# Optimization experiments

Hardware: AMD Instinct MI355X
Metric: run time of the kernel (lower is better)

Reference implementation:

```python
import jax, jax.numpy as jnp
import numpy as np

B = 32768      # batch
S = 512        # state_dim
G = 128        # goal_dim
A = 32         # action_dim
P = 16         # num_primitives
H1, H2 = 512, 256        # big_model hidden sizes
VH1, VH2 = 1024, 512     # value hidden sizes


def _w(k, shape, scale=0.05):
    return jax.random.normal(k, shape, jnp.float32) * scale


def setup_inputs() -> dict:
    key = jax.random.key(0)
    ks = jax.random.split(key, 24)
    d = {"features": jax.random.normal(ks[0], (B, S + G), jnp.float32)}
    # state encoder: S->H1->H2
    d["se_w1"] = _w(ks[1], (S, H1));  d["se_b1"] = jnp.zeros((H1,), jnp.float32)
    d["se_w2"] = _w(ks[2], (H1, H2)); d["se_b2"] = jnp.zeros((H2,), jnp.float32)
    # goal encoder: G->H1->H2
    d["ge_w1"] = _w(ks[3], (G, H1));  d["ge_b1"] = jnp.zeros((H1,), jnp.float32)
    d["ge_w2"] = _w(ks[4], (H1, H2)); d["ge_b2"] = jnp.zeros((H2,), jnp.float32)
    # gate: 2*H2->H2->P (sigmoid)
    d["gt_w1"] = _w(ks[5], (2 * H2, H2)); d["gt_b1"] = jnp.zeros((H2,), jnp.float32)
    d["gt_w2"] = _w(ks[6], (H2, P));      d["gt_b2"] = jnp.zeros((P,), jnp.float32)
    # primitive state encoder: S->H1->H2
    d["pse_w1"] = _w(ks[7], (S, H1));  d["pse_b1"] = jnp.zeros((H1,), jnp.float32)
    d["pse_w2"] = _w(ks[8], (H1, H2)); d["pse_b2"] = jnp.zeros((H2,), jnp.float32)
    # P primitives, each H2->H2->2A (stacked for batched GEMM)
    d["pw1"] = _w(ks[9], (P, H2, H2));     d["pb1"] = jnp.zeros((P, H2), jnp.float32)
    d["pw2"] = _w(ks[10], (P, H2, 2 * A)); d["pb2"] = jnp.zeros((P, 2 * A), jnp.float32)
    # value net: (S+G)->VH1->VH2
    d["vf_w1"] = _w(ks[11], (S + G, VH1)); d["vf_b1"] = jnp.zeros((VH1,), jnp.float32)
    d["vf_w2"] = _w(ks[12], (VH1, VH2));   d["vf_b2"] = jnp.zeros((VH2,), jnp.float32)
    return d


def _mlp2(x, w1, b1, w2, b2):
    return jax.nn.relu(jax.nn.relu(x @ w1 + b1) @ w2 + b2)


def reference(features,
              se_w1, se_b1, se_w2, se_b2,
              ge_w1, ge_b1, ge_w2, ge_b2,
              gt_w1, gt_b1, gt_w2, gt_b2,
              pse_w1, pse_b1, pse_w2, pse_b2,
              pw1, pb1, pw2, pb2,
              vf_w1, vf_b1, vf_w2, vf_b2):
    state, goal = features[:, :S], features[:, S:]
    # gating weights
    s_emb = _mlp2(state, se_w1, se_b1, se_w2, se_b2)      # [B,H2]
    g_emb = _mlp2(goal, ge_w1, ge_b1, ge_w2, ge_b2)       # [B,H2]
    gate_in = jnp.concatenate([s_emb, g_emb], axis=-1)    # [B,2*H2]
    weights = jax.nn.sigmoid(jax.nn.relu(gate_in @ gt_w1 + gt_b1) @ gt_w2 + gt_b2)  # [B,P]
    # shared primitive embedding
    prim_embed = _mlp2(state, pse_w1, pse_b1, pse_w2, pse_b2)  # [B,H2]
    # all primitives as one batched GEMM
    h = jax.nn.relu(jnp.einsum('bh,phk->bpk', prim_embed, pw1) + pb1[None])  # [B,P,H2]
    out = jnp.einsum('bpk,pkd->bpd', h, pw2) + pb2[None]                      # [B,P,2A]
    mu, log_std = out[..., :A], out[..., A:]
    sigma = jnp.exp(log_std)
    # precision-weighted Gaussian mixture
    inv = weights[..., None] / sigma        # [B,P,A]
    denom = inv.sum(axis=1)                 # [B,A]
    mean = (inv * mu).sum(axis=1) / denom   # [B,A]  (learn_log_std=True -> mean only)
    # critic
    value = _mlp2(features, vf_w1, vf_b1, vf_w2, vf_b2)  # [B,VH2]
    return (mean, value)
```

## Files before the change

kernel.cpp:

```cpp
#include <hip/hip_runtime.h>
#include <stdint.h>

#define NB 32768

typedef __bf16 bf16x8 __attribute__((ext_vector_type(8)));
typedef float f32x4 __attribute__((ext_vector_type(4)));

__device__ __forceinline__ unsigned pack_bf2(float a, float b) {
  union { __bf16 h[2]; unsigned u; } t;
  t.h[0] = (__bf16)a; t.h[1] = (__bf16)b;
  return t.u;
}
__device__ __forceinline__ unsigned short bf16b(float f) {
  union { __bf16 h; unsigned short u; } t;
  t.h = (__bf16)f;
  return t.u;
}
__device__ __forceinline__ float bf2f(unsigned short h) {
  union { unsigned u; float f; } v; v.u = ((unsigned)h) << 16;
  return v.f;
}

__device__ __forceinline__ void gld_lds16(void* lds, const void* g) {
  __builtin_amdgcn_global_load_lds(
      (__attribute__((address_space(1))) unsigned int*)(uintptr_t)g,
      (__attribute__((address_space(3))) unsigned int*)(uintptr_t)lds,
      16, 0, 0);
}

__device__ __forceinline__ int xcd_swz(int bid, int nwg) {
  return (bid & 7) * (nwg >> 3) + (bid >> 3);
}


__global__ __launch_bounds__(256) void fconv_k(const float* __restrict__ src,
                                               unsigned short* __restrict__ dst) {
  size_t idx = ((size_t)blockIdx.x * 256 + threadIdx.x) * 8;
  float4 a = *(const float4*)(src + idx);
  float4 b = *(const float4*)(src + idx + 4);
  uint4 o;
  o.x = pack_bf2(a.x, a.y); o.y = pack_bf2(a.z, a.w);
  o.z = pack_bf2(b.x, b.y); o.w = pack_bf2(b.z, b.w);
  *(uint4*)(dst + idx) = o;
}

__global__ __launch_bounds__(256) void bcat_k(const float* __restrict__ a,
                                              const float* __restrict__ b,
                                              float* __restrict__ dst) {
  const int i = blockIdx.x * 256 + threadIdx.x;
  dst[i] = (i < 512) ? a[i] : b[i - 512];
}

struct TJobs {
  const float* src[11];
  unsigned short* dst[11];
  int K[11], N[11], batch[11];
};

__global__ __launch_bounds__(256) void wtrans_k(TJobs jobs) {
  const int job = blockIdx.y;
  const int K = jobs.K[job], N = jobs.N[job];
  const int KT = K >> 5, NT = N >> 5;
  const int ntiles = jobs.batch[job] * KT * NT;
  const int t = blockIdx.x;
  if (t >= ntiles) return;
  const int b = t / (KT * NT);
  const int rem = t - b * KT * NT;
  const int kt = rem / NT, nt = rem - kt * NT;
  const float* src = jobs.src[job] + (size_t)b * K * N;
  unsigned short* dst = jobs.dst[job] + (size_t)b * K * N;
  __shared__ float tile[32][33];
  const int i = threadIdx.x >> 5, jj = threadIdx.x & 31;
#pragma unroll
  for (int s = 0; s < 4; ++s)
    tile[i + 8 * s][jj] = src[(size_t)(kt * 32 + i + 8 * s) * N + nt * 32 + jj];
  __syncthreads();
#pragma unroll
  for (int s = 0; s < 4; ++s)
    dst[(size_t)(nt * 32 + i + 8 * s) * K + kt * 32 + jj] = bf16b(tile[jj][i + 8 * s]);
}


template <bool OUT_BF16>
__global__ __launch_bounds__(256, 2) void gemm2_k(const unsigned short* __restrict__ A, int lda,
                                                  const unsigned short* __restrict__ WT,
                                                  const float* __restrict__ bias,
                                                  void* __restrict__ Cout, int ldc, int K,
                                                  int ncl2) {
  __shared__ unsigned short a_s[2][128 * 32];
  __shared__ unsigned short b_s[2][256 * 32];
  const int tid = threadIdx.x;
  const int l = tid & 63, w = tid >> 6;
  const int lr = l & 15, lq = l >> 4;
  const int wg = xcd_swz(blockIdx.x, gridDim.x);
  const int col0 = (wg & ((1 << ncl2) - 1)) << 8;
  const int row0 = (wg >> ncl2) << 7;
  const int wbase = tid & ~63;

  auto stage = [&](int buf, int t) {
    const int k0 = t << 5;
#pragma unroll
    for (int i = 0; i < 2; ++i) {
      const int s = i * 256 + tid;
      const int r = s >> 2, c = s & 3;
      const int cs = c ^ ((r >> 1) & 3);
      gld_lds16(&a_s[buf][(size_t)(i * 256 + wbase) * 8],
                A + (size_t)(row0 + r) * lda + k0 + cs * 8);
    }
#pragma unroll
    for (int i = 0; i < 4; ++i) {
      const int s = i * 256 + tid;
      const int n = s >> 2, c = s & 3;
      const int cs = c ^ ((n >> 1) & 3);
      gld_lds16(&b_s[buf][(size_t)(i * 256 + wbase) * 8],
                WT + (size_t)(col0 + n) * K + k0 + cs * 8);
    }
  };

  f32x4 acc[8][4] = {};
  const int nt = K >> 5;
  stage(0, 0);
  __syncthreads();
#pragma unroll 1
  for (int t = 0; t < nt; ++t) {
    const int cur = t & 1;
    if (t + 1 < nt) stage(cur ^ 1, t + 1);
    bf16x8 av[8], bv[4];
#pragma unroll
    for (int mf = 0; mf < 8; ++mf) {
      const int r = mf * 16 + lr;
      av[mf] = *(const bf16x8*)&a_s[cur][r * 32 + ((lq ^ ((r >> 1) & 3)) << 3)];
    }
#pragma unroll
    for (int nf = 0; nf < 4; ++nf) {
      const int n = w * 64 + nf * 16 + lr;
      bv[nf] = *(const bf16x8*)&b_s[cur][n * 32 + ((lq ^ ((n >> 1) & 3)) << 3)];
    }
#pragma unroll
    for (int mf = 0; mf < 8; ++mf)
#pragma unroll
      for (int nf = 0; nf < 4; ++nf)
        acc[mf][nf] = __builtin_amdgcn_mfma_f32_16x16x32_bf16(av[mf], bv[nf], acc[mf][nf], 0, 0, 0);
    __syncthreads();
  }

#pragma unroll
  for (int nf = 0; nf < 4; ++nf) {
    const int gc = col0 + w * 64 + nf * 16 + lr;
    const float bb = bias[gc];
#pragma unroll
    for (int mf = 0; mf < 8; ++mf) {
      const int gr = row0 + mf * 16 + (lq << 2);
#pragma unroll
      for (int r = 0; r < 4; ++r) {
        float v = acc[mf][nf][r] + bb;
        v = fmaxf(v, 0.0f);
        if (OUT_BF16)
          ((unsigned short*)Cout)[(size_t)(gr + r) * ldc + gc] = bf16b(v);
        else
          ((float*)Cout)[(size_t)(gr + r) * ldc + gc] = v;
      }
    }
  }
}


template <bool OUT_BF16>
__global__ __launch_bounds__(256, 2) void gemm3_k(const unsigned short* __restrict__ A, int lda,
                                                  const unsigned short* __restrict__ WT,
                                                  const float* __restrict__ bias,
                                                  void* __restrict__ Cout, int ldc, int K,
                                                  int ncl2) {
  __shared__ unsigned short a_s[2][128 * 32];
  __shared__ unsigned short b_s[2][128 * 32];
  const int tid = threadIdx.x;
  const int l = tid & 63, w = tid >> 6;
  const int wm = w >> 1, wn = w & 1;
  const int lr = l & 15, lq = l >> 4;
  const int wg = xcd_swz(blockIdx.x, gridDim.x);
  const int col0 = (wg & ((1 << ncl2) - 1)) << 7;
  const int row0 = (wg >> ncl2) << 7;
  const int wbase = tid & ~63;

  auto stage = [&](int buf, int t) {
    const int k0 = t << 5;
#pragma unroll
    for (int i = 0; i < 2; ++i) {
      const int s = i * 256 + tid;
      const int r = s >> 2, c = s & 3;
      const int cs = c ^ ((r >> 1) & 3);
      gld_lds16(&a_s[buf][(size_t)(i * 256 + wbase) * 8],
                A + (size_t)(row0 + r) * lda + k0 + cs * 8);
    }
#pragma unroll
    for (int i = 0; i < 2; ++i) {
      const int s = i * 256 + tid;
      const int n = s >> 2, c = s & 3;
      const int cs = c ^ ((n >> 1) & 3);
      gld_lds16(&b_s[buf][(size_t)(i * 256 + wbase) * 8],
                WT + (size_t)(col0 + n) * K + k0 + cs * 8);
    }
  };

  f32x4 acc[4][4] = {};
  const int nt = K >> 5;
  stage(0, 0);
  __syncthreads();
#pragma unroll 1
  for (int t = 0; t < nt; ++t) {
    const int cur = t & 1;
    if (t + 1 < nt) stage(cur ^ 1, t + 1);
    bf16x8 av[4], bv[4];
#pragma unroll
    for (int mf = 0; mf < 4; ++mf) {
      const int r = wm * 64 + mf * 16 + lr;
      av[mf] = *(const bf16x8*)&a_s[cur][r * 32 + ((lq ^ ((r >> 1) & 3)) << 3)];
    }
#pragma unroll
    for (int nf = 0; nf < 4; ++nf) {
      const int n = wn * 64 + nf * 16 + lr;
      bv[nf] = *(const bf16x8*)&b_s[cur][n * 32 + ((lq ^ ((n >> 1) & 3)) << 3)];
    }
#pragma unroll
    for (int mf = 0; mf < 4; ++mf)
#pragma unroll
      for (int nf = 0; nf < 4; ++nf)
        acc[mf][nf] = __builtin_amdgcn_mfma_f32_16x16x32_bf16(av[mf], bv[nf], acc[mf][nf], 0, 0, 0);
    __syncthreads();
  }

#pragma unroll
  for (int nf = 0; nf < 4; ++nf) {
    const int gc = col0 + wn * 64 + nf * 16 + lr;
    const float bb = bias[gc];
#pragma unroll
    for (int mf = 0; mf < 4; ++mf) {
      const int gr = row0 + wm * 64 + mf * 16 + (lq << 2);
#pragma unroll
      for (int r = 0; r < 4; ++r) {
        float v = acc[mf][nf][r] + bb;
        v = fmaxf(v, 0.0f);
        if (OUT_BF16)
          ((unsigned short*)Cout)[(size_t)(gr + r) * ldc + gc] = bf16b(v);
        else
          ((float*)Cout)[(size_t)(gr + r) * ldc + gc] = v;
      }
    }
  }
}


__global__ __launch_bounds__(256) void gt2_k(const unsigned short* __restrict__ gate_h,
                                             const float* __restrict__ w2,
                                             const float* __restrict__ b2,
                                             float* __restrict__ wgt) {
  __shared__ float w_s[256 * 16];
  __shared__ unsigned short a_s[16 * 264];
  const int tid = threadIdx.x;
  const int row0 = blockIdx.x * 16;
  for (int i = tid; i < 256 * 16; i += 256) w_s[i] = w2[i];
  for (int i = tid; i < 512; i += 256) {
    const int r = i >> 5, cg = i & 31;
    *(uint4*)&a_s[r * 264 + cg * 8] =
        *(const uint4*)(gate_h + (size_t)(row0 + r) * 256 + cg * 8);
  }
  __syncthreads();
  const int rr = tid >> 4, col = tid & 15;
  float sum = b2[col];
#pragma unroll 8
  for (int k = 0; k < 256; ++k)
    sum += bf2f(a_s[rr * 264 + k]) * w_s[k * 16 + col];
  wgt[(size_t)(row0 + rr) * 16 + col] = 1.0f / (1.0f + __expf(-sum));
}


__global__ __launch_bounds__(512, 4) void prim_head_k(
    const unsigned short* __restrict__ prim,
    const float* __restrict__ wgt,
    const unsigned short* __restrict__ pw1t,
    const float* __restrict__ pb1,
    const unsigned short* __restrict__ pw2t,
    const float* __restrict__ pb2,
    unsigned short* __restrict__ outbuf)
{
  __shared__ unsigned short prim_s[2][128 * 32];
  __shared__ unsigned short w1_s[2][128 * 32];
  __shared__ unsigned short h_s[128 * 128];
  __shared__ unsigned short pw2_s[64 * 128];
  const int tid = threadIdx.x;
  const int l = tid & 63;
  const int w = tid >> 6;
  const int lr = l & 15, lq = l >> 4;
  const int wn2 = w & 1, wr2 = w >> 1;
  const int row0 = blockIdx.x << 7;
  const int p = blockIdx.y;
  const int wbase = tid & ~63;

  const unsigned short* w1p = pw1t + (size_t)p * 65536;
  const unsigned short* w2p = pw2t + (size_t)p * 16384;

  auto stage_ab = [&](int t) {
    const int buf = t & 1;
    const int k0 = (t & 7) << 5;
    const int nb2 = (t >> 3) << 7;
    const int rw = tid >> 2, kc = tid & 3;
    const int kcs = kc ^ ((rw >> 1) & 3);
    gld_lds16(&prim_s[buf][(size_t)wbase * 8],
              prim + (size_t)(row0 + rw) * 256 + k0 + kcs * 8);
    gld_lds16(&w1_s[buf][(size_t)wbase * 8],
              w1p + (size_t)(nb2 + rw) * 256 + k0 + kcs * 8);
  };
  auto stage_pw2 = [&](int half) {
    const int nbase = half << 7;
#pragma unroll
    for (int i = 0; i < 2; ++i) {
      const int c = i * 512 + tid;
      const int d = c >> 4, kc = c & 15;
      gld_lds16(&pw2_s[(size_t)(i * 512 + wbase) * 8],
                w2p + (size_t)d * 256 + nbase + ((kc ^ (d & 7)) << 3));
    }
  };

  stage_ab(0);
  stage_pw2(0);

  f32x4 acc2[2][2] = {};

  for (int half = 0; half < 2; ++half) {
    float4 pb1v[4];
#pragma unroll
    for (int nf = 0; nf < 4; ++nf)
      pb1v[nf] = *(const float4*)(pb1 + p * 256 + (half << 7) + wn2 * 64 + nf * 16 + (lq << 2));

    f32x4 acc1[4][2] = {};
#pragma unroll 1
    for (int ks = 0; ks < 8; ++ks) {
      const int t = (half << 3) + ks;
      const int cur = t & 1;
      asm volatile("s_waitcnt vmcnt(0)" ::: "memory");
      __builtin_amdgcn_s_barrier();
      if (t < 15) stage_ab(t + 1);
      bf16x8 av[4], bv[2];
#pragma unroll
      for (int nf = 0; nf < 4; ++nf) {
        const int n = wn2 * 64 + nf * 16 + lr;
        av[nf] = *(const bf16x8*)&w1_s[cur][n * 32 + ((lq ^ ((n >> 1) & 3)) << 3)];
      }
#pragma unroll
      for (int rf = 0; rf < 2; ++rf) {
        const int r = wr2 * 32 + rf * 16 + lr;
        bv[rf] = *(const bf16x8*)&prim_s[cur][r * 32 + ((lq ^ ((r >> 1) & 3)) << 3)];
      }
#pragma unroll
      for (int nf = 0; nf < 4; ++nf)
#pragma unroll
        for (int rf = 0; rf < 2; ++rf)
          acc1[nf][rf] = __builtin_amdgcn_mfma_f32_16x16x32_bf16(av[nf], bv[rf], acc1[nf][rf], 0, 0, 0);
    }

#pragma unroll
    for (int nf = 0; nf < 4; ++nf) {
      const int n0 = wn2 * 64 + nf * 16 + (lq << 2);
      const float4 bb = pb1v[nf];
#pragma unroll
      for (int rf = 0; rf < 2; ++rf) {
        const int row = wr2 * 32 + rf * 16 + lr;
        uint2 pk;
        pk.x = pack_bf2(fmaxf(acc1[nf][rf][0] + bb.x, 0.0f),
                        fmaxf(acc1[nf][rf][1] + bb.y, 0.0f));
        pk.y = pack_bf2(fmaxf(acc1[nf][rf][2] + bb.z, 0.0f),
                        fmaxf(acc1[nf][rf][3] + bb.w, 0.0f));
        *(uint2*)&h_s[row * 128 + (((n0 >> 3) ^ (row & 7)) << 3) + (n0 & 7)] = pk;
      }
    }
    asm volatile("s_waitcnt lgkmcnt(0)" ::: "memory");
    __builtin_amdgcn_s_barrier();

    {
      const int dmu = wn2 * 16;
      const int row_a = wr2 * 32;
#pragma unroll
      for (int kc8 = 0; kc8 < 4; ++kc8) {
        const int slot = ((kc8 << 2) + lq) ^ (lr & 7);
        const bf16x8 amu = *(const bf16x8*)&pw2_s[(dmu + lr) * 128 + (slot << 3)];
        const bf16x8 als = *(const bf16x8*)&pw2_s[(dmu + 32 + lr) * 128 + (slot << 3)];
        const bf16x8 b0 = *(const bf16x8*)&h_s[(row_a + lr) * 128 + (slot << 3)];
        const bf16x8 b1 = *(const bf16x8*)&h_s[(row_a + 16 + lr) * 128 + (slot << 3)];
        acc2[0][0] = __builtin_amdgcn_mfma_f32_16x16x32_bf16(amu, b0, acc2[0][0], 0, 0, 0);
        acc2[0][1] = __builtin_amdgcn_mfma_f32_16x16x32_bf16(als, b0, acc2[0][1], 0, 0, 0);
        acc2[1][0] = __builtin_amdgcn_mfma_f32_16x16x32_bf16(amu, b1, acc2[1][0], 0, 0, 0);
        acc2[1][1] = __builtin_amdgcn_mfma_f32_16x16x32_bf16(als, b1, acc2[1][1], 0, 0, 0);
      }
    }
    asm volatile("s_waitcnt lgkmcnt(0)" ::: "memory");
    __builtin_amdgcn_s_barrier();
    if (half == 0) stage_pw2(1);
  }

  {
    const int dmu = wn2 * 16;
    const int row_a = wr2 * 32;
    const int d0 = dmu + (lq << 2);
    const float4 b2mu = *(const float4*)(pb2 + p * 64 + d0);
    const float4 b2ls = *(const float4*)(pb2 + p * 64 + 32 + d0);
    const float wp0 = wgt[(size_t)(row0 + row_a + lr) * 16 + p];
    const float wp1 = wgt[(size_t)(row0 + row_a + 16 + lr) * 16 + p];
#pragma unroll
    for (int s = 0; s < 2; ++s) {
      const int row_g = row0 + row_a + s * 16 + lr;
      const float wp = s ? wp1 : wp0;
      unsigned short* ob = outbuf + ((size_t)row_g * 16 + p) * 64;
      const float mu0 = acc2[s][0][0] + b2mu.x, ls0 = acc2[s][1][0] + b2ls.x;
      const float mu1 = acc2[s][0][1] + b2mu.y, ls1 = acc2[s][1][1] + b2ls.y;
      const float mu2 = acc2[s][0][2] + b2mu.z, ls2 = acc2[s][1][2] + b2ls.z;
      const float mu3 = acc2[s][0][3] + b2mu.w, ls3 = acc2[s][1][3] + b2ls.w;
      const float iv0 = wp * __expf(-ls0), iv1 = wp * __expf(-ls1);
      const float iv2 = wp * __expf(-ls2), iv3 = wp * __expf(-ls3);
      uint2 nmp, ivp;
      nmp.x = pack_bf2(iv0 * mu0, iv1 * mu1);
      nmp.y = pack_bf2(iv2 * mu2, iv3 * mu3);
      ivp.x = pack_bf2(iv0, iv1);
      ivp.y = pack_bf2(iv2, iv3);
      *(uint2*)(ob + d0) = nmp;
      *(uint2*)(ob + 32 + d0) = ivp;
    }
  }
}


__global__ __launch_bounds__(256) void mix_finish_k(const unsigned short* __restrict__ buf,
                                                    float* __restrict__ mean_out) {
  const int gid = blockIdx.x * 256 + threadIdx.x;
  const int row = gid >> 3;
  const int a0 = (gid & 7) * 4;
  const unsigned short* rp = buf + (size_t)row * 1024;
  float nx = 0, ny = 0, nz = 0, nw = 0, dx = 0, dy = 0, dz = 0, dw = 0;
#pragma unroll
  for (int p = 0; p < 16; ++p) {
    const uint2 m = *(const uint2*)(rp + p * 64 + a0);
    const uint2 v = *(const uint2*)(rp + p * 64 + 32 + a0);
    nx += bf2f((unsigned short)(m.x & 0xffff)); ny += bf2f((unsigned short)(m.x >> 16));
    nz += bf2f((unsigned short)(m.y & 0xffff)); nw += bf2f((unsigned short)(m.y >> 16));
    dx += bf2f((unsigned short)(v.x & 0xffff)); dy += bf2f((unsigned short)(v.x >> 16));
    dz += bf2f((unsigned short)(v.y & 0xffff)); dw += bf2f((unsigned short)(v.y >> 16));
  }
  float4 res;
  res.x = nx / dx; res.y = ny / dy; res.z = nz / dz; res.w = nw / dw;
  *(float4*)(mean_out + (size_t)row * 32 + a0) = res;
}


extern "C" void kernel_launch(void* const* d_in, const int* in_sizes, int n_in,
                              void* d_out, int out_size, void* d_ws, size_t ws_size,
                              hipStream_t stream) {
  const float* features = (const float*)d_in[0];
  const float* se_w1 = (const float*)d_in[1];
  const float* se_b1 = (const float*)d_in[2];
  const float* se_w2 = (const float*)d_in[3];
  const float* se_b2 = (const float*)d_in[4];
  const float* ge_w1 = (const float*)d_in[5];
  const float* ge_b1 = (const float*)d_in[6];
  const float* ge_w2 = (const float*)d_in[7];
  const float* ge_b2 = (const float*)d_in[8];
  const float* gt_w1 = (const float*)d_in[9];
  const float* gt_b1 = (const float*)d_in[10];
  const float* gt_w2 = (const float*)d_in[11];
  const float* gt_b2 = (const float*)d_in[12];
  const float* pse_w1 = (const float*)d_in[13];
  const float* pse_b1 = (const float*)d_in[14];
  const float* pse_w2 = (const float*)d_in[15];
  const float* pse_b2 = (const float*)d_in[16];
  const float* pw1 = (const float*)d_in[17];
  const float* pb1 = (const float*)d_in[18];
  const float* pw2 = (const float*)d_in[19];
  const float* pb2 = (const float*)d_in[20];
  const float* vf_w1 = (const float*)d_in[21];
  const float* vf_b1 = (const float*)d_in[22];
  const float* vf_w2 = (const float*)d_in[23];
  const float* vf_b2 = (const float*)d_in[24];
  (void)in_sizes; (void)n_in; (void)out_size; (void)ws_size;

  char* base = (char*)d_ws;
  size_t off = 0;
  auto alloc = [&](size_t bytes) -> char* {
    char* p = base + off;
    off += (bytes + 255) & ~(size_t)255;
    return p;
  };
  unsigned short* fbf     = (unsigned short*)alloc((size_t)NB * 640 * 2);
  unsigned short* bufA    = (unsigned short*)alloc((size_t)NB * 1024 * 2);
  unsigned short* g1      = (unsigned short*)alloc((size_t)NB * 512 * 2);
  unsigned short* gate_in = (unsigned short*)alloc((size_t)NB * 512 * 2);
  unsigned short* gate_h  = (unsigned short*)alloc((size_t)NB * 256 * 2);
  unsigned short* prim    = (unsigned short*)alloc((size_t)NB * 256 * 2);
  float* wgt              = (float*)alloc((size_t)NB * 16 * 4);
  unsigned short* wcat1t  = (unsigned short*)alloc((size_t)1024 * 512 * 2);
  float* bcat1            = (float*)alloc(1024 * 4);
  unsigned short* se_w2t  = (unsigned short*)alloc(256 * 512 * 2);
  unsigned short* ge_w1t  = (unsigned short*)alloc(512 * 128 * 2);
  unsigned short* ge_w2t  = (unsigned short*)alloc(256 * 512 * 2);
  unsigned short* gt_w1t  = (unsigned short*)alloc(256 * 512 * 2);
  unsigned short* pse_w2t = (unsigned short*)alloc(256 * 512 * 2);
  unsigned short* pw1t    = (unsigned short*)alloc((size_t)16 * 256 * 256 * 2);
  unsigned short* pw2t    = (unsigned short*)alloc((size_t)16 * 64 * 256 * 2);
  unsigned short* vf_w1t  = (unsigned short*)alloc(1024 * 640 * 2);
  unsigned short* vf_w2t  = (unsigned short*)alloc(512 * 1024 * 2);

  unsigned short* se_w1t  = wcat1t;
  unsigned short* pse_w1t = wcat1t + 512 * 512;

  unsigned short* outbuf = (unsigned short*)bufA;

  float* mean_out = (float*)d_out;
  float* value_out = (float*)d_out + (size_t)NB * 32;

  fconv_k<<<dim3(10240), dim3(256), 0, stream>>>(features, fbf);
  bcat_k<<<dim3(4), dim3(256), 0, stream>>>(se_b1, pse_b1, bcat1);

  TJobs jobs;
  auto setj = [&](int i, const float* s, unsigned short* d, int K, int N, int b) {
    jobs.src[i] = s; jobs.dst[i] = d; jobs.K[i] = K; jobs.N[i] = N; jobs.batch[i] = b;
  };
  setj(0, se_w1, se_w1t, 512, 512, 1);
  setj(1, se_w2, se_w2t, 512, 256, 1);
  setj(2, ge_w1, ge_w1t, 128, 512, 1);
  setj(3, ge_w2, ge_w2t, 512, 256, 1);
  setj(4, gt_w1, gt_w1t, 512, 256, 1);
  setj(5, pse_w1, pse_w1t, 512, 512, 1);
  setj(6, pse_w2, pse_w2t, 512, 256, 1);
  setj(7, pw1, pw1t, 256, 256, 16);
  setj(8, pw2, pw2t, 256, 64, 16);
  setj(9, vf_w1, vf_w1t, 640, 1024, 1);
  setj(10, vf_w2, vf_w2t, 1024, 512, 1);
  wtrans_k<<<dim3(1024, 11), dim3(256), 0, stream>>>(jobs);

  gemm2_k<true><<<dim3(1024), dim3(256), 0, stream>>>(fbf, 640, wcat1t, bcat1, bufA, 1024, 512, 2);
  gemm2_k<true><<<dim3(512), dim3(256), 0, stream>>>(fbf + 512, 640, ge_w1t, ge_b1, g1, 512, 128, 1);
  gemm3_k<true><<<dim3(512), dim3(256), 0, stream>>>(bufA, 1024, se_w2t, se_b2, gate_in, 512, 512, 1);
  gemm3_k<true><<<dim3(512), dim3(256), 0, stream>>>(g1, 512, ge_w2t, ge_b2, gate_in + 256, 512, 512, 1);
  gemm3_k<true><<<dim3(512), dim3(256), 0, stream>>>(gate_in, 512, gt_w1t, gt_b1, gate_h, 256, 512, 1);
  gt2_k<<<dim3(2048), dim3(256), 0, stream>>>(gate_h, gt_w2, gt_b2, wgt);
  gemm3_k<true><<<dim3(512), dim3(256), 0, stream>>>(bufA + 512, 1024, pse_w2t, pse_b2, prim, 256, 512, 1);
  gemm2_k<true><<<dim3(1024), dim3(256), 0, stream>>>(fbf, 640, vf_w1t, vf_b1, bufA, 1024, 640, 2);
  gemm2_k<false><<<dim3(512), dim3(256), 0, stream>>>(bufA, 1024, vf_w2t, vf_b2, value_out, 512, 1024, 1);
  prim_head_k<<<dim3(256, 16), dim3(512), 0, stream>>>(prim, wgt, pw1t, pb1, pw2t, pb2, outbuf);
  mix_finish_k<<<dim3(1024), dim3(256), 0, stream>>>(outbuf, mean_out);
}
```

Measured before the change: 440.3 us.

## Keep prim activations in registers and triple-buffer W1 tiles in LDS

Each wave now loads its slice of the primitive embedding straight from global memory into registers once, instead of staging it through LDS at every k-step. Only the W1 tile is staged through LDS, now with three buffers and a prefetch distance of two, using finer vmcnt waits. The intent is to cut LDS traffic and barrier stalls and to overlap global loads with the MFMAs better. The cost is higher register pressure (16 bf16x8 vectors held per lane) and full unrolling of the loops, which may reduce occupancy at 512 threads with launch bounds of 4.

```diff
diff --git a/kernel.cpp b/kernel.cpp
--- a/kernel.cpp
+++ b/kernel.cpp
@@ -283,8 +283,7 @@
     const float* __restrict__ pb2,
     unsigned short* __restrict__ outbuf)
 {
-  __shared__ unsigned short prim_s[2][128 * 32];
-  __shared__ unsigned short w1_s[2][128 * 32];
+  __shared__ unsigned short w1_s[3][128 * 32];
   __shared__ unsigned short h_s[128 * 128];
   __shared__ unsigned short pw2_s[64 * 128];
   const int tid = threadIdx.x;
@@ -299,16 +298,14 @@
   const unsigned short* w1p = pw1t + (size_t)p * 65536;
   const unsigned short* w2p = pw2t + (size_t)p * 16384;
 
-  auto stage_ab = [&](int t) {
-    const int buf = t & 1;
+  auto stage_w1 = [&](int t) {
+    const int buf = t % 3;
     const int k0 = (t & 7) << 5;
-    const int nb2 = (t >> 3) << 7;
-    const int rw = tid >> 2, kc = tid & 3;
-    const int kcs = kc ^ ((rw >> 1) & 3);
-    gld_lds16(&prim_s[buf][(size_t)wbase * 8],
-              prim + (size_t)(row0 + rw) * 256 + k0 + kcs * 8);
+    const int nb2 = ((t >> 3) & 1) << 7;
+    const int n = tid >> 2, kc = tid & 3;
+    const int kcs = kc ^ ((n >> 1) & 3);
     gld_lds16(&w1_s[buf][(size_t)wbase * 8],
-              w1p + (size_t)(nb2 + rw) * 256 + k0 + kcs * 8);
+              w1p + (size_t)(nb2 + n) * 256 + k0 + kcs * 8);
   };
   auto stage_pw2 = [&](int half) {
     const int nbase = half << 7;
@@ -321,47 +318,53 @@
     }
   };
 
-  stage_ab(0);
   stage_pw2(0);
 
+  bf16x8 pf[8][2];
+#pragma unroll
+  for (int kq = 0; kq < 8; ++kq)
+#pragma unroll
+    for (int rf = 0; rf < 2; ++rf)
+      pf[kq][rf] = *(const bf16x8*)(prim +
+          (size_t)(row0 + wr2 * 32 + rf * 16 + lr) * 256 + kq * 32 + lq * 8);
+#pragma unroll
+  for (int kq = 0; kq < 8; ++kq)
+    asm volatile("" :: "v"(pf[kq][0]), "v"(pf[kq][1]));
+
+  stage_w1(0);
+  stage_w1(1);
+
   f32x4 acc2[2][2] = {};
 
+#pragma unroll
   for (int half = 0; half < 2; ++half) {
-    float4 pb1v[4];
-#pragma unroll
-    for (int nf = 0; nf < 4; ++nf)
-      pb1v[nf] = *(const float4*)(pb1 + p * 256 + (half << 7) + wn2 * 64 + nf * 16 + (lq << 2));
-
     f32x4 acc1[4][2] = {};
-#pragma unroll 1
+#pragma unroll
     for (int ks = 0; ks < 8; ++ks) {
-      const int t = (half << 3) + ks;
-      const int cur = t & 1;
-      asm volatile("s_waitcnt vmcnt(0)" ::: "memory");
+      const int t = half * 8 + ks;
+      if (t == 8 || t == 9)      asm volatile("s_waitcnt vmcnt(3)" ::: "memory");
+      else if (t == 15)          asm volatile("s_waitcnt vmcnt(0)" ::: "memory");
+      else                       asm volatile("s_waitcnt vmcnt(1)" ::: "memory");
       __builtin_amdgcn_s_barrier();
-      if (t < 15) stage_ab(t + 1);
-      bf16x8 av[4], bv[2];
+      if (t < 14) stage_w1(t + 2);
+      bf16x8 av[4];
 #pragma unroll
       for (int nf = 0; nf < 4; ++nf) {
         const int n = wn2 * 64 + nf * 16 + lr;
-        av[nf] = *(const bf16x8*)&w1_s[cur][n * 32 + ((lq ^ ((n >> 1) & 3)) << 3)];
+        av[nf] = *(const bf16x8*)&w1_s[t % 3][n * 32 + ((lq ^ ((n >> 1) & 3)) << 3)];
       }
 #pragma unroll
-      for (int rf = 0; rf < 2; ++rf) {
-        const int r = wr2 * 32 + rf * 16 + lr;
-        bv[rf] = *(const bf16x8*)&prim_s[cur][r * 32 + ((lq ^ ((r >> 1) & 3)) << 3)];
-      }
-#pragma unroll
       for (int nf = 0; nf < 4; ++nf)
 #pragma unroll
         for (int rf = 0; rf < 2; ++rf)
-          acc1[nf][rf] = __builtin_amdgcn_mfma_f32_16x16x32_bf16(av[nf], bv[rf], acc1[nf][rf], 0, 0, 0);
+          acc1[nf][rf] = __builtin_amdgcn_mfma_f32_16x16x32_bf16(av[nf], pf[ks][rf],
+                                                                 acc1[nf][rf], 0, 0, 0);
     }
 
 #pragma unroll
     for (int nf = 0; nf < 4; ++nf) {
       const int n0 = wn2 * 64 + nf * 16 + (lq << 2);
-      const float4 bb = pb1v[nf];
+      const float4 bb = *(const float4*)(pb1 + p * 256 + (half << 7) + n0);
 #pragma unroll
       for (int rf = 0; rf < 2; ++rf) {
         const int row = wr2 * 32 + rf * 16 + lr;
```

Result: slower. 491.9 us (+11.7%).
